# Performance work log

Hardware: AMD Instinct MI355X
Metric: run time of the kernel (lower is better)

## Reference

```python
import jax, jax.numpy as jnp
from jax import lax
import numpy as np
import math

N, T, H, PD = 1024, 32, 256, 256
E, DT, SD = 2 * H, H // 16, 16  # mamba expand, dt_rank, state_dim
TAU = 1.0

def _xavier(k, shape):
    s = math.sqrt(6.0 / (shape[0] + shape[1]))
    return jax.random.uniform(k, shape, minval=-s, maxval=s, dtype=jnp.float32)

def setup_inputs() -> dict:
    key = jax.random.key(0)
    ks = jax.random.split(key, 40)
    adj = (jax.random.uniform(ks[0], (T, N, N)) < 0.02).astype(jnp.float32)
    p = {
        'adj': adj,
        # input SpatialLayer (pos_dim -> H)
        'msg1_w': _xavier(ks[1], (PD, H)), 'msg1_b': jnp.zeros(H),
        'upd1_w': _xavier(ks[2], (PD + H, H)), 'upd1_b': jnp.zeros(H),
        'ln1_g': jnp.ones(H), 'ln1_b': jnp.zeros(H),
        # second SpatialLayer (H -> H)
        'msg2_w': _xavier(ks[3], (H, H)), 'msg2_b': jnp.zeros(H),
        'upd2_w': _xavier(ks[4], (2 * H, H)), 'upd2_b': jnp.zeros(H),
        'ln2_g': jnp.ones(H), 'ln2_b': jnp.zeros(H),
        # MambaBlock
        'mb_ln_g': jnp.ones(H), 'mb_ln_b': jnp.zeros(H),
        'in_w': _xavier(ks[5], (H, 2 * E)), 'in_b': jnp.zeros(2 * E),
        'delta_w': _xavier(ks[6], (E, DT)), 'delta_b': jnp.zeros(DT),
        'dt_w': _xavier(ks[7], (DT, E)), 'dt_b': jnp.zeros(E),
        'Bp_w': _xavier(ks[8], (E, SD)), 'Bp_b': jnp.zeros(SD),
        'Cp_w': _xavier(ks[9], (E, SD)), 'Cp_b': jnp.zeros(SD),
        'A_log': -jnp.exp(0.1 * jax.random.normal(ks[10], (E, SD))),
        'D_vec': jnp.zeros(E),
        'out_w': _xavier(ks[11], (E, H)), 'out_b': jnp.zeros(H),
        # LateEdgeGateHead
        'q_w': _xavier(ks[12], (H, H)), 'k_w': _xavier(ks[13], (H, H)),
        'gate_bias': jnp.float32(-1.0),
    }
    return p

def _layernorm(x, g, b, eps=1e-5):
    mu = jnp.mean(x, -1, keepdims=True)
    var = jnp.mean(jnp.square(x - mu), -1, keepdims=True)
    return (x - mu) / jnp.sqrt(var + eps) * g + b

def _sincos_pe(n, d):
    pos = jnp.arange(n, dtype=jnp.float32)[:, None]
    div = jnp.exp(jnp.arange(0, d, 2, dtype=jnp.float32) * (-math.log(10000.0) / d))
    ang = pos * div  # [n, d/2]
    return jnp.stack([jnp.sin(ang), jnp.cos(ang)], axis=-1).reshape(n, d)

def reference(adj, msg1_w, msg1_b, upd1_w, upd1_b, ln1_g, ln1_b,
              msg2_w, msg2_b, upd2_w, upd2_b, ln2_g, ln2_b,
              mb_ln_g, mb_ln_b, in_w, in_b, delta_w, delta_b, dt_w, dt_b,
              Bp_w, Bp_b, Cp_w, Cp_b, A_log, D_vec, out_w, out_b,
              q_w, k_w, gate_bias):
    pe = _sincos_pe(N, PD)  # [N, PD]
    # --- spatial layer 1 (shared pe across time) ---
    m1 = pe @ msg1_w + msg1_b                                   # [N, H]
    agg1 = jnp.einsum('tij,jh->tih', adj, m1)                   # [T, N, H]
    x = jnp.concatenate([jnp.broadcast_to(pe, (T, N, PD)), agg1], -1)
    x = _layernorm(jax.nn.relu(x @ upd1_w + upd1_b), ln1_g, ln1_b)
    # --- spatial layer 2 ---
    m2 = x @ msg2_w + msg2_b
    agg2 = jnp.einsum('tij,tjh->tih', adj, m2)
    x = jnp.concatenate([x, agg2], -1)
    x = _layernorm(jax.nn.relu(x @ upd2_w + upd2_b), ln2_g, ln2_b)  # [T, N, H]
    # --- Mamba over time, batch = nodes ---
    seq = jnp.transpose(x, (1, 0, 2))                           # [N, T, H]
    res = seq
    xn = _layernorm(seq, mb_ln_g, mb_ln_b)
    xp = xn @ in_w + in_b
    x1, gate = jnp.split(xp, 2, axis=-1)                        # [N, T, E] each
    x1 = jax.nn.silu(x1)
    delta = jax.nn.softplus((x1 @ delta_w + delta_b) @ dt_w + dt_b)  # [N, T, E]
    Bm = x1 @ Bp_w + Bp_b                                       # [N, T, SD]
    Cm = x1 @ Cp_w + Cp_b
    A = -jnp.exp(A_log)                                         # [E, SD]
    def step(h, inp):
        xt, dt_, bt, ct = inp                                   # [N,E],[N,E],[N,SD],[N,SD]
        A_disc = jnp.exp(dt_[:, :, None] * A)                   # [N, E, SD]
        h = A_disc * h + dt_[:, :, None] * bt[:, None, :] * xt[:, :, None]
        yt = jnp.sum(ct[:, None, :] * h, -1)                    # [N, E]
        return h, yt
    h0 = jnp.zeros((N, E, SD), dtype=seq.dtype)
    xs = (jnp.swapaxes(x1, 0, 1), jnp.swapaxes(delta, 0, 1),
          jnp.swapaxes(Bm, 0, 1), jnp.swapaxes(Cm, 0, 1))
    _, ys = lax.scan(step, h0, xs)                              # [T, N, E]
    y = jnp.swapaxes(ys, 0, 1) + x1 * D_vec
    y = y * jax.nn.silu(gate)
    mb_out = y @ out_w + out_b + res                            # [N, T, H]
    outs = jnp.transpose(mb_out, (1, 0, 2))                     # [T, N, H]
    # --- late gate head per timestep ---
    q = outs @ q_w
    k = outs @ k_w
    scores = jnp.einsum('tnh,tmh->tnm', q, k) / (math.sqrt(H) * max(TAU, 1e-6))
    logits = scores + gate_bias
    probs = jax.nn.sigmoid(logits)
    return outs, probs, logits
```

## Files before the change

### kernel.cpp

```cpp
#include <hip/hip_runtime.h>
#include <hip/hip_bf16.h>

typedef __hip_bfloat16 bf16;
typedef short s16x8 __attribute__((ext_vector_type(8)));
typedef float f32x4 __attribute__((ext_vector_type(4)));

#define T_  32
#define N_  1024
#define H_  256
#define E_  512
#define SD_ 16

static const long MBYTE = 1024L * 1024L;

__device__ __forceinline__ float b2f(bf16 v){ return __bfloat162float(v); }
__device__ __forceinline__ bf16  f2b(float v){ return __float2bfloat16(v); }
__device__ __forceinline__ void  stf(bf16* p, float v){ *p = f2b(v); }
__device__ __forceinline__ void  stf(float* p, float v){ *p = v; }

#define G2L16(gp, lp) __builtin_amdgcn_global_load_lds( \
    (const __attribute__((address_space(1))) void*)(const void*)(gp), \
    (__attribute__((address_space(3))) void*)(void*)(lp), 16, 0, 0)

struct TDesc { const float* src; int K; int N; bf16* dst; int ldT; };
struct PrepArgs {
    TDesc t[13];
    bf16* pe;
    const float* pa; const float* pb; const float* pc; float* po;
};

__global__ __launch_bounds__(256) void prep_kernel(PrepArgs P){
    int z = blockIdx.z;
    int tid = threadIdx.x;
    if (z < 13) {
        const TDesc d = P.t[z];
        int k0 = blockIdx.x * 32, n0 = blockIdx.y * 32;
        if (k0 >= d.K || n0 >= d.N) return;
        __shared__ float S[32][33];
        int r = tid >> 3, c4 = (tid & 7) * 4;
        #pragma unroll
        for (int u = 0; u < 4; ++u) {
            int k = k0 + r, n = n0 + c4 + u;
            S[r][c4 + u] = (k < d.K && n < d.N) ? d.src[(long)k * d.N + n] : 0.0f;
        }
        __syncthreads();
        int n = n0 + (tid >> 3);
        #pragma unroll
        for (int u = 0; u < 4; ++u) {
            int k = k0 + (tid & 7) * 4 + u;
            if (n < d.N && k < d.K) d.dst[(long)n * d.ldT + k] = f2b(S[(tid & 7) * 4 + u][tid >> 3]);
        }
    } else if (z == 13) {
        int n = blockIdx.y * 32 + blockIdx.x;
        int dd = tid;
        int i2 = (dd >> 1) * 2;
        float div = __expf((float)i2 * (-9.210340371976184f / 256.0f));
        float ang = (float)n * div;
        P.pe[n * 256 + dd] = f2b((dd & 1) ? __cosf(ang) : __sinf(ang));
    } else {
        if (blockIdx.x || blockIdx.y) return;
        if (tid < 16) P.po[tid] = P.pa[tid];
        else if (tid < 32) P.po[tid] = P.pb[tid - 16];
        else if (tid < 48) P.po[tid] = P.pc[tid - 32];
    }
}

template<int OP>
__global__ __launch_bounds__(256) void mfma_gemm128(
    const bf16* __restrict__ A, int lda,
    const bf16* BT0, const bf16* BT1, int ldbt0, int ldbt1,
    float* Cf0, float* Cf1, bf16* Cb0, bf16* Cb1, int ldc,
    int K, const float* bias0, const float* bias1, const float* res)
{
    int z = blockIdx.z;
    const bf16* BT = z ? BT1 : BT0;
    int ldbt = z ? ldbt1 : ldbt0;
    float* Cf = z ? Cf1 : Cf0;
    bf16*  Cb = z ? Cb1 : Cb0;
    const float* bias = z ? bias1 : bias0;

    __shared__ short As[4096];
    __shared__ short Bs[4096];
    int tid = threadIdx.x;
    int w = tid >> 6, l = tid & 63;
    int wr = w >> 1, wc = w & 1;
    long row0 = (long)blockIdx.y * 128, col0 = (long)blockIdx.x * 128;
    const short* Ag = (const short*)A + row0 * lda;
    const short* Bg = (const short*)BT + col0 * ldbt;
    int sr = w * 16 + (l >> 2);
    int sc = (l & 3) * 8;
    short* lA = As + w * 512 + l * 8;
    short* lB = Bs + w * 512 + l * 8;
    f32x4 acc[4][4] = {};
    for (int k0 = 0; k0 < K; k0 += 32) {
        G2L16(Ag + (long)sr * lda + k0 + sc, lA);
        G2L16(Ag + (long)(sr + 64) * lda + k0 + sc, lA + 2048);
        G2L16(Bg + (long)sr * ldbt + k0 + sc, lB);
        G2L16(Bg + (long)(sr + 64) * ldbt + k0 + sc, lB + 2048);
        __syncthreads();
        s16x8 af[4], bf[4];
        #pragma unroll
        for (int f = 0; f < 4; ++f) {
            af[f] = *(const s16x8*)&As[(wr * 64 + f * 16 + (l & 15)) * 32 + (l >> 4) * 8];
            bf[f] = *(const s16x8*)&Bs[(wc * 64 + f * 16 + (l & 15)) * 32 + (l >> 4) * 8];
        }
        #pragma unroll
        for (int fm = 0; fm < 4; ++fm)
            #pragma unroll
            for (int fn = 0; fn < 4; ++fn)
                acc[fm][fn] = __builtin_amdgcn_mfma_f32_16x16x32_bf16(af[fm], bf[fn], acc[fm][fn], 0, 0, 0);
        __syncthreads();
    }
    #pragma unroll
    for (int fm = 0; fm < 4; ++fm) {
        int er = (int)row0 + wr * 64 + fm * 16 + (l >> 4) * 4;
        #pragma unroll
        for (int fn = 0; fn < 4; ++fn) {
            int ec = (int)col0 + wc * 64 + fn * 16 + (l & 15);
            float bb = bias ? bias[ec] : 0.0f;
            #pragma unroll
            for (int rg = 0; rg < 4; ++rg) {
                long idx = (long)(er + rg) * ldc + ec;
                float v = acc[fm][fn][rg] + bb;
                if (res) v += res[idx];
                if (OP == 1) v = v / (1.0f + __expf(-v));
                if (Cf) Cf[idx] = v;
                if (Cb) Cb[idx] = f2b(v);
            }
        }
    }
}

__global__ __launch_bounds__(256) void score_mfma128(
    const bf16* __restrict__ Q, const bf16* __restrict__ Km,
    float* __restrict__ probs, float* __restrict__ logits,
    const float* __restrict__ gbp)
{
    int t = blockIdx.z;
    const short* Ag = (const short*)(Q  + (long)t * N_ * 256) + (long)blockIdx.y * 128 * 256;
    const short* Bg = (const short*)(Km + (long)t * N_ * 256) + (long)blockIdx.x * 128 * 256;
    __shared__ short As[4096];
    __shared__ short Bs[4096];
    int tid = threadIdx.x;
    int w = tid >> 6, l = tid & 63;
    int wr = w >> 1, wc = w & 1;
    int sr = w * 16 + (l >> 2);
    int sc = (l & 3) * 8;
    short* lA = As + w * 512 + l * 8;
    short* lB = Bs + w * 512 + l * 8;
    f32x4 acc[4][4] = {};
    for (int k0 = 0; k0 < 256; k0 += 32) {
        G2L16(Ag + (long)sr * 256 + k0 + sc, lA);
        G2L16(Ag + (long)(sr + 64) * 256 + k0 + sc, lA + 2048);
        G2L16(Bg + (long)sr * 256 + k0 + sc, lB);
        G2L16(Bg + (long)(sr + 64) * 256 + k0 + sc, lB + 2048);
        __syncthreads();
        s16x8 af[4], bf[4];
        #pragma unroll
        for (int f = 0; f < 4; ++f) {
            af[f] = *(const s16x8*)&As[(wr * 64 + f * 16 + (l & 15)) * 32 + (l >> 4) * 8];
            bf[f] = *(const s16x8*)&Bs[(wc * 64 + f * 16 + (l & 15)) * 32 + (l >> 4) * 8];
        }
        #pragma unroll
        for (int fm = 0; fm < 4; ++fm)
            #pragma unroll
            for (int fn = 0; fn < 4; ++fn)
                acc[fm][fn] = __builtin_amdgcn_mfma_f32_16x16x32_bf16(af[fm], bf[fn], acc[fm][fn], 0, 0, 0);
        __syncthreads();
    }
    float gb = gbp[0];
    long tbase = (long)t * N_ * N_;
    int row0 = blockIdx.y * 128, col0 = blockIdx.x * 128;
    #pragma unroll
    for (int fm = 0; fm < 4; ++fm) {
        int er = row0 + wr * 64 + fm * 16 + (l >> 4) * 4;
        #pragma unroll
        for (int fn = 0; fn < 4; ++fn) {
            int ec = col0 + wc * 64 + fn * 16 + (l & 15);
            #pragma unroll
            for (int rg = 0; rg < 4; ++rg) {
                float zz = acc[fm][fn][rg] * 0.0625f + gb;
                long idx = tbase + (long)(er + rg) * N_ + ec;
                logits[idx] = zz;
                probs[idx]  = 1.0f / (1.0f + __expf(-zz));
            }
        }
    }
}

__global__ __launch_bounds__(256) void mfma_gemm64(
    const bf16* __restrict__ A, int lda,
    const bf16* __restrict__ BT, int ldbt,
    float* __restrict__ Cf, int ldc,
    int M, int N, int K, const float* __restrict__ bias)
{
    __shared__ short As[64][40];
    __shared__ short Bs[64][40];
    int tid = threadIdx.x;
    int w = tid >> 6, l = tid & 63;
    int row0 = blockIdx.y * 64, col0 = blockIdx.x * 64;
    int sr = tid >> 2, sk = (tid & 3) * 8;
    const short* Ag = (const short*)A;
    const short* Bg = (const short*)BT;
    f32x4 acc[4] = {};
    for (int k0 = 0; k0 < K; k0 += 32) {
        *(s16x8*)&As[sr][sk] = *(const s16x8*)(Ag + (long)(row0 + sr) * lda + k0 + sk);
        int bn = col0 + sr;
        s16x8 bv = {};
        if (bn < N) bv = *(const s16x8*)(Bg + (long)bn * ldbt + k0 + sk);
        *(s16x8*)&Bs[sr][sk] = bv;
        __syncthreads();
        s16x8 a = *(const s16x8*)&As[w * 16 + (l & 15)][(l >> 4) * 8];
        #pragma unroll
        for (int ct = 0; ct < 4; ++ct) {
            s16x8 b = *(const s16x8*)&Bs[ct * 16 + (l & 15)][(l >> 4) * 8];
            acc[ct] = __builtin_amdgcn_mfma_f32_16x16x32_bf16(a, b, acc[ct], 0, 0, 0);
        }
        __syncthreads();
    }
    int er = row0 + w * 16 + (l >> 4) * 4;
    int ec = l & 15;
    #pragma unroll
    for (int ct = 0; ct < 4; ++ct) {
        int gc = col0 + ct * 16 + ec;
        if (gc >= N) continue;
        float bb = bias ? bias[gc] : 0.0f;
        #pragma unroll
        for (int rg = 0; rg < 4; ++rg)
            Cf[(long)(er + rg) * ldc + gc] = acc[ct][rg] + bb;
    }
}

__global__ __launch_bounds__(256) void idx_build(
    const float* __restrict__ adj, unsigned short* __restrict__ IDX, int* __restrict__ CNT)
{
    int r = blockIdx.x;
    const float* arow = adj + ((long)r << 10);
    __shared__ int wcnt[4];
    int tid = threadIdx.x, wv = tid >> 6, lane = tid & 63;
    int total = 0;
    unsigned short* out = IDX + (long)r * 128;
    #pragma unroll
    for (int u = 0; u < 4; ++u) {
        float av = arow[u * 256 + tid];
        unsigned long long mask = __ballot(av != 0.0f);
        if (lane == 0) wcnt[wv] = __popcll(mask);
        __syncthreads();
        int base = total;
        for (int w2 = 0; w2 < wv; ++w2) base += wcnt[w2];
        if (av != 0.0f) {
            int pos = base + __popcll(mask & ((1ull << lane) - 1ull));
            if (pos < 128) out[pos] = (unsigned short)(u * 256 + tid);
        }
        total += wcnt[0] + wcnt[1] + wcnt[2] + wcnt[3];
        __syncthreads();
    }
    if (tid == 0) CNT[r] = total < 128 ? total : 128;
}

__global__ __launch_bounds__(256) void agg_gather(
    const unsigned short* __restrict__ IDX, const int* __restrict__ CNT,
    const bf16* __restrict__ Bm, long tstride,
    bf16* __restrict__ out, int old, int ooff)
{
    int r = blockIdx.x;
    int t = r >> 10;
    const bf16* B = Bm + (long)t * tstride;
    __shared__ unsigned short sidx[128];
    int tid = threadIdx.x;
    int cnt = CNT[r];
    if (tid < 128) sidx[tid] = IDX[(long)r * 128 + tid];
    __syncthreads();
    float acc = 0.0f;
    for (int k = 0; k < cnt; ++k)
        acc += b2f(B[(long)sidx[k] * 256 + tid]);
    out[(long)r * old + ooff + tid] = f2b(acc);
}

__global__ __launch_bounds__(256) void row_ln1(
    const float* __restrict__ in, const float* __restrict__ addf,
    const float* __restrict__ g, const float* __restrict__ b,
    bf16* __restrict__ out, int rows)
{
    int wv = threadIdx.x >> 6, lane = threadIdx.x & 63;
    int row = blockIdx.x * 4 + wv;
    if (row >= rows) return;
    const float* p = in + (long)row * 256 + lane * 4;
    const float* q = addf + (long)(row & 1023) * 256 + lane * 4;
    float v[4];
    #pragma unroll
    for (int u = 0; u < 4; ++u) v[u] = fmaxf(p[u] + q[u], 0.0f);
    float s = v[0] + v[1] + v[2] + v[3];
    #pragma unroll
    for (int o = 32; o >= 1; o >>= 1) s += __shfl_xor(s, o, 64);
    float mu = s * (1.0f / 256.0f);
    float d0 = v[0]-mu, d1 = v[1]-mu, d2 = v[2]-mu, d3 = v[3]-mu;
    float sq = d0*d0 + d1*d1 + d2*d2 + d3*d3;
    #pragma unroll
    for (int o = 32; o >= 1; o >>= 1) sq += __shfl_xor(sq, o, 64);
    float rs = rsqrtf(sq * (1.0f / 256.0f) + 1e-5f);
    bf16* o = out + (long)row * 512 + lane * 4;
    #pragma unroll
    for (int u = 0; u < 4; ++u)
        o[u] = f2b((v[u] - mu) * rs * g[lane * 4 + u] + b[lane * 4 + u]);
}

__global__ __launch_bounds__(256) void dbl_ln(
    const float* __restrict__ in,
    const float* __restrict__ g2, const float* __restrict__ b2,
    const float* __restrict__ gm, const float* __restrict__ bm,
    float* __restrict__ X2f, bf16* __restrict__ XNb, int rows)
{
    int wv = threadIdx.x >> 6, lane = threadIdx.x & 63;
    int row = blockIdx.x * 4 + wv;
    if (row >= rows) return;
    const float* p = in + (long)row * 256 + lane * 4;
    float v[4];
    #pragma unroll
    for (int u = 0; u < 4; ++u) v[u] = fmaxf(p[u], 0.0f);
    float s = v[0] + v[1] + v[2] + v[3];
    #pragma unroll
    for (int o = 32; o >= 1; o >>= 1) s += __shfl_xor(s, o, 64);
    float mu = s * (1.0f / 256.0f);
    float sq = 0.0f;
    #pragma unroll
    for (int u = 0; u < 4; ++u) { float d = v[u] - mu; sq += d * d; }
    #pragma unroll
    for (int o = 32; o >= 1; o >>= 1) sq += __shfl_xor(sq, o, 64);
    float rs = rsqrtf(sq * (1.0f / 256.0f) + 1e-5f);
    float o1[4];
    float* qx = X2f + (long)row * 256 + lane * 4;
    #pragma unroll
    for (int u = 0; u < 4; ++u) {
        o1[u] = (v[u] - mu) * rs * g2[lane * 4 + u] + b2[lane * 4 + u];
        qx[u] = o1[u];
    }
    float s2 = o1[0] + o1[1] + o1[2] + o1[3];
    #pragma unroll
    for (int o = 32; o >= 1; o >>= 1) s2 += __shfl_xor(s2, o, 64);
    float mu2 = s2 * (1.0f / 256.0f);
    float sq2 = 0.0f;
    #pragma unroll
    for (int u = 0; u < 4; ++u) { float d = o1[u] - mu2; sq2 += d * d; }
    #pragma unroll
    for (int o = 32; o >= 1; o >>= 1) sq2 += __shfl_xor(sq2, o, 64);
    float rs2 = rsqrtf(sq2 * (1.0f / 256.0f) + 1e-5f);
    bf16* qn = XNb + (long)row * 256 + lane * 4;
    #pragma unroll
    for (int u = 0; u < 4; ++u)
        qn[u] = f2b((o1[u] - mu2) * rs2 * gm[lane * 4 + u] + bm[lane * 4 + u]);
}

__global__ __launch_bounds__(512) void scan2(
    const bf16* __restrict__ X1,
    bf16* __restrict__ G,
    const float* __restrict__ DBC,
    const bf16* __restrict__ DTwT,
    const float* __restrict__ DTb,
    const float* __restrict__ A_log,
    const float* __restrict__ D_vec)
{
    int n = blockIdx.x;
    int e = threadIdx.x;
    float A[SD_], wdt[SD_];
    #pragma unroll
    for (int s = 0; s < SD_; ++s) A[s] = -__expf(A_log[e * SD_ + s]);
    #pragma unroll
    for (int s = 0; s < SD_; ++s) wdt[s] = b2f(DTwT[e * SD_ + s]);
    float dtb = DTb[e];
    float Dv = D_vec[e];
    float h[SD_];
    #pragma unroll
    for (int s = 0; s < SD_; ++s) h[s] = 0.0f;
    for (int t = 0; t < T_; ++t) {
        long row = (long)t * N_ + n;
        const float* dbc = DBC + row * 48;
        float z = dtb;
        #pragma unroll
        for (int k = 0; k < SD_; ++k) z += dbc[k] * wdt[k];
        float dt = (z > 15.0f) ? z : __logf(1.0f + __expf(z));
        float x1 = b2f(X1[row * (long)E_ + e]);
        float gv = b2f(G[row * (long)E_ + e]);
        float dx = dt * x1;
        float yv = 0.0f;
        #pragma unroll
        for (int s = 0; s < SD_; ++s) {
            h[s] = __expf(dt * A[s]) * h[s] + dx * dbc[16 + s];
            yv += dbc[32 + s] * h[s];
        }
        G[row * (long)E_ + e] = f2b((yv + x1 * Dv) * gv);
    }
}

extern "C" void kernel_launch(void* const* d_in, const int* in_sizes, int n_in,
                              void* d_out, int out_size, void* d_ws, size_t ws_size,
                              hipStream_t stream)
{
    if (ws_size < (size_t)(212 * MBYTE)) return;
    if (n_in != 32 || in_sizes[0] != T_ * N_ * N_ || in_sizes[15] != 256 * 1024) return;

    const float* adj = (const float*)d_in[0];
    const float* P1w = (const float*)d_in[1];
    const float* P1b = (const float*)d_in[2];
    const float* U1w = (const float*)d_in[3];
    const float* U1b = (const float*)d_in[4];
    const float* L1g = (const float*)d_in[5];
    const float* L1b = (const float*)d_in[6];
    const float* P2w = (const float*)d_in[7];
    const float* P2b = (const float*)d_in[8];
    const float* U2w = (const float*)d_in[9];
    const float* U2b = (const float*)d_in[10];
    const float* L2g = (const float*)d_in[11];
    const float* L2b = (const float*)d_in[12];
    const float* MBg = (const float*)d_in[13];
    const float* MBb = (const float*)d_in[14];
    const float* INw = (const float*)d_in[15];
    const float* INb = (const float*)d_in[16];
    const float* DLw = (const float*)d_in[17];
    const float* DLb = (const float*)d_in[18];
    const float* DTw = (const float*)d_in[19];
    const float* DTb = (const float*)d_in[20];
    const float* BPw = (const float*)d_in[21];
    const float* BPb = (const float*)d_in[22];
    const float* CPw = (const float*)d_in[23];
    const float* CPb = (const float*)d_in[24];
    const float* ALg = (const float*)d_in[25];
    const float* DV  = (const float*)d_in[26];
    const float* OWw = (const float*)d_in[27];
    const float* OWb = (const float*)d_in[28];
    const float* QWw = (const float*)d_in[29];
    const float* KWw = (const float*)d_in[30];
    const float* GB  = (const float*)d_in[31];

    char* w = (char*)d_ws;
    float* R0    = (float*)(w + 0);
    bf16*  XCATb = (bf16*)(w + 32 * MBYTE);
    bf16*  AGG1b = (bf16*)(w + 64 * MBYTE);
    bf16*  M2b   = (bf16*)(w + 64 * MBYTE);
    bf16*  OUTb  = (bf16*)(w + 64 * MBYTE);
    bf16*  X1b   = (bf16*)(w + 80 * MBYTE);
    bf16*  Gb    = (bf16*)(w + 112 * MBYTE);
    float* X2f   = (float*)(w + 144 * MBYTE);
    bf16*  Qb    = (bf16*)(w + 144 * MBYTE);
    bf16*  Kb    = (bf16*)(w + 160 * MBYTE);
    bf16*  XNb   = (bf16*)(w + 176 * MBYTE);
    float* DBC   = (float*)(w + 192 * MBYTE);
    unsigned short* IDX = (unsigned short*)(w + 198 * MBYTE);
    int*   CNT   = (int*)(w + 206 * MBYTE);
    float* BASE1 = (float*)(w + 207 * MBYTE);
    bf16*  PEb   = (bf16*)(w + 208 * MBYTE);
    bf16*  M1b   = (bf16*)(w + 208 * MBYTE + 524288);
    bf16*  WT    = (bf16*)(w + 209 * MBYTE);
    float* B48   = (float*)(w + 211 * MBYTE);

    bf16* P1wT  = WT + 0;
    bf16* U1wT  = WT + 65536;
    bf16* P2wT  = WT + 196608;
    bf16* U2wT  = WT + 262144;
    bf16* INwT  = WT + 393216;
    bf16* DTwT  = WT + 655360;
    bf16* OWwT  = WT + 663552;
    bf16* QWwT  = WT + 794624;
    bf16* KWwT  = WT + 860160;
    bf16* DBCwT = WT + 925696;

    float* out0       = (float*)d_out;
    float* out_probs  = out0 + (long)T_ * N_ * H_;
    float* out_logits = out_probs + (long)T_ * N_ * N_;

    const int RN = T_ * N_;
    dim3 blk(256);
    const float* fnull = nullptr;
    float* f32null = nullptr;
    bf16*  b16null = nullptr;

    PrepArgs P;
    P.t[0]  = {P1w, 256, 256,  P1wT, 256};
    P.t[1]  = {U1w, 512, 256,  U1wT, 512};
    P.t[2]  = {P2w, 256, 256,  P2wT, 256};
    P.t[3]  = {U2w, 512, 256,  U2wT, 512};
    P.t[4]  = {INw, 256, 1024, INwT, 256};
    P.t[5]  = {DTw, 16,  512,  DTwT, 16};
    P.t[6]  = {OWw, 512, 256,  OWwT, 512};
    P.t[7]  = {QWw, 256, 256,  QWwT, 256};
    P.t[8]  = {KWw, 256, 256,  KWwT, 256};
    P.t[9]  = {DLw, 512, 16,   DBCwT, 512};
    P.t[10] = {BPw, 512, 16,   DBCwT + 16 * 512, 512};
    P.t[11] = {CPw, 512, 16,   DBCwT + 32 * 512, 512};
    P.t[12] = {DLw, 1,   1,    DBCwT, 512};
    P.pe = PEb; P.pa = DLb; P.pb = BPb; P.pc = CPb; P.po = B48;
    hipLaunchKernelGGL(prep_kernel, dim3(32, 32, 15), blk, 0, stream, P);
    hipLaunchKernelGGL(idx_build, dim3(RN), blk, 0, stream, adj, IDX, CNT);

    hipLaunchKernelGGL((mfma_gemm128<0>), dim3(2, 8, 2), blk, 0, stream,
                       PEb, 256, P1wT, U1wT, 256, 512,
                       f32null, BASE1, M1b, b16null, 256, 256, P1b, U1b, fnull);

    hipLaunchKernelGGL(agg_gather, dim3(RN), blk, 0, stream, IDX, CNT, M1b, 0L, AGG1b, 256, 0);

    hipLaunchKernelGGL((mfma_gemm128<0>), dim3(2, 256, 1), blk, 0, stream,
                       AGG1b, 256, U1wT + 256, U1wT + 256, 512, 512,
                       R0, f32null, b16null, b16null, 256, 256, fnull, fnull, fnull);
    hipLaunchKernelGGL(row_ln1, dim3(RN / 4), blk, 0, stream, R0, BASE1, L1g, L1b, XCATb, RN);

    hipLaunchKernelGGL((mfma_gemm128<0>), dim3(2, 256, 1), blk, 0, stream,
                       XCATb, 512, P2wT, P2wT, 256, 256,
                       f32null, f32null, M2b, b16null, 256, 256, P2b, fnull, fnull);

    hipLaunchKernelGGL(agg_gather, dim3(RN), blk, 0, stream, IDX, CNT, M2b,
                       (long)N_ * 256, XCATb, 512, 256);

    hipLaunchKernelGGL((mfma_gemm128<0>), dim3(2, 256, 1), blk, 0, stream,
                       XCATb, 512, U2wT, U2wT, 512, 512,
                       R0, f32null, b16null, b16null, 256, 512, U2b, fnull, fnull);
    hipLaunchKernelGGL(dbl_ln, dim3(RN / 4), blk, 0, stream,
                       R0, L2g, L2b, MBg, MBb, X2f, XNb, RN);

    hipLaunchKernelGGL((mfma_gemm128<1>), dim3(4, 256, 2), blk, 0, stream,
                       XNb, 256, INwT, INwT + 512 * 256, 256, 256,
                       f32null, f32null, X1b, Gb, 512, 256, INb, INb + 512, fnull);

    hipLaunchKernelGGL(mfma_gemm64, dim3(1, 512), blk, 0, stream,
                       X1b, 512, DBCwT, 512, DBC, 48, RN, 48, 512, B48);

    hipLaunchKernelGGL(scan2, dim3(N_), dim3(512), 0, stream,
                       X1b, Gb, DBC, DTwT, DTb, ALg, DV);

    hipLaunchKernelGGL((mfma_gemm128<0>), dim3(2, 256, 1), blk, 0, stream,
                       Gb, 512, OWwT, OWwT, 512, 512,
                       out0, f32null, OUTb, b16null, 256, 512, OWb, fnull, X2f);

    hipLaunchKernelGGL((mfma_gemm128<0>), dim3(2, 256, 2), blk, 0, stream,
                       OUTb, 256, QWwT, KWwT, 256, 256,
                       f32null, f32null, Qb, Kb, 256, 256, fnull, fnull, fnull);

    hipLaunchKernelGGL(score_mfma128, dim3(8, 8, T_), blk, 0, stream,
                       Qb, Kb, out_probs, out_logits, GB);
}
```

Before: 582.3 us.

## Merge index build into prep kernel, unroll gather, use nontemporal logit stores

```diff
diff --git a/kernel.cpp b/kernel.cpp
--- a/kernel.cpp
+++ b/kernel.cpp
@@ -15,8 +15,6 @@
 
 __device__ __forceinline__ float b2f(bf16 v){ return __bfloat162float(v); }
 __device__ __forceinline__ bf16  f2b(float v){ return __float2bfloat16(v); }
-__device__ __forceinline__ void  stf(bf16* p, float v){ *p = f2b(v); }
-__device__ __forceinline__ void  stf(float* p, float v){ *p = v; }
 
 #define G2L16(gp, lp) __builtin_amdgcn_global_load_lds( \
     (const __attribute__((address_space(1))) void*)(const void*)(gp), \
@@ -27,6 +25,7 @@
     TDesc t[13];
     bf16* pe;
     const float* pa; const float* pb; const float* pc; float* po;
+    const float* adj; unsigned short* IDX; int* CNT;
 };
 
 __global__ __launch_bounds__(256) void prep_kernel(PrepArgs P){
@@ -57,11 +56,34 @@
         float div = __expf((float)i2 * (-9.210340371976184f / 256.0f));
         float ang = (float)n * div;
         P.pe[n * 256 + dd] = f2b((dd & 1) ? __cosf(ang) : __sinf(ang));
-    } else {
+    } else if (z == 14) {
         if (blockIdx.x || blockIdx.y) return;
         if (tid < 16) P.po[tid] = P.pa[tid];
         else if (tid < 32) P.po[tid] = P.pb[tid - 16];
         else if (tid < 48) P.po[tid] = P.pc[tid - 32];
+    } else {
+        int r = (z - 15) * 1024 + blockIdx.y * 32 + blockIdx.x;
+        const float* arow = P.adj + ((long)r << 10);
+        __shared__ int wcnt[4];
+        int wv = tid >> 6, lane = tid & 63;
+        int total = 0;
+        unsigned short* out = P.IDX + (long)r * 128;
+        #pragma unroll
+        for (int u = 0; u < 4; ++u) {
+            float av = arow[u * 256 + tid];
+            unsigned long long mask = __ballot(av != 0.0f);
+            if (lane == 0) wcnt[wv] = __popcll(mask);
+            __syncthreads();
+            int base = total;
+            for (int w2 = 0; w2 < wv; ++w2) base += wcnt[w2];
+            if (av != 0.0f) {
+                int pos = base + __popcll(mask & ((1ull << lane) - 1ull));
+                if (pos < 128) out[pos] = (unsigned short)(u * 256 + tid);
+            }
+            total += wcnt[0] + wcnt[1] + wcnt[2] + wcnt[3];
+            __syncthreads();
+        }
+        if (tid == 0) P.CNT[r] = total < 128 ? total : 128;
     }
 }
 
@@ -181,8 +203,8 @@
             for (int rg = 0; rg < 4; ++rg) {
                 float zz = acc[fm][fn][rg] * 0.0625f + gb;
                 long idx = tbase + (long)(er + rg) * N_ + ec;
-                logits[idx] = zz;
-                probs[idx]  = 1.0f / (1.0f + __expf(-zz));
+                __builtin_nontemporal_store(zz, &logits[idx]);
+                __builtin_nontemporal_store(1.0f / (1.0f + __expf(-zz)), &probs[idx]);
             }
         }
     }
@@ -231,33 +253,6 @@
     }
 }
 
-__global__ __launch_bounds__(256) void idx_build(
-    const float* __restrict__ adj, unsigned short* __restrict__ IDX, int* __restrict__ CNT)
-{
-    int r = blockIdx.x;
-    const float* arow = adj + ((long)r << 10);
-    __shared__ int wcnt[4];
-    int tid = threadIdx.x, wv = tid >> 6, lane = tid & 63;
-    int total = 0;
-    unsigned short* out = IDX + (long)r * 128;
-    #pragma unroll
-    for (int u = 0; u < 4; ++u) {
-        float av = arow[u * 256 + tid];
-        unsigned long long mask = __ballot(av != 0.0f);
-        if (lane == 0) wcnt[wv] = __popcll(mask);
-        __syncthreads();
-        int base = total;
-        for (int w2 = 0; w2 < wv; ++w2) base += wcnt[w2];
-        if (av != 0.0f) {
-            int pos = base + __popcll(mask & ((1ull << lane) - 1ull));
-            if (pos < 128) out[pos] = (unsigned short)(u * 256 + tid);
-        }
-        total += wcnt[0] + wcnt[1] + wcnt[2] + wcnt[3];
-        __syncthreads();
-    }
-    if (tid == 0) CNT[r] = total < 128 ? total : 128;
-}
-
 __global__ __launch_bounds__(256) void agg_gather(
     const unsigned short* __restrict__ IDX, const int* __restrict__ CNT,
     const bf16* __restrict__ Bm, long tstride,
@@ -271,10 +266,17 @@
     int cnt = CNT[r];
     if (tid < 128) sidx[tid] = IDX[(long)r * 128 + tid];
     __syncthreads();
-    float acc = 0.0f;
-    for (int k = 0; k < cnt; ++k)
-        acc += b2f(B[(long)sidx[k] * 256 + tid]);
-    out[(long)r * old + ooff + tid] = f2b(acc);
+    float a0 = 0.0f, a1 = 0.0f, a2 = 0.0f, a3 = 0.0f;
+    int k = 0;
+    for (; k + 4 <= cnt; k += 4) {
+        float v0 = b2f(B[(long)sidx[k]     * 256 + tid]);
+        float v1 = b2f(B[(long)sidx[k + 1] * 256 + tid]);
+        float v2 = b2f(B[(long)sidx[k + 2] * 256 + tid]);
+        float v3 = b2f(B[(long)sidx[k + 3] * 256 + tid]);
+        a0 += v0; a1 += v1; a2 += v2; a3 += v3;
+    }
+    for (; k < cnt; ++k) a0 += b2f(B[(long)sidx[k] * 256 + tid]);
+    out[(long)r * old + ooff + tid] = f2b((a0 + a1) + (a2 + a3));
 }
 
 __global__ __launch_bounds__(256) void row_ln1(
@@ -489,8 +491,8 @@
     P.t[11] = {CPw, 512, 16,   DBCwT + 32 * 512, 512};
     P.t[12] = {DLw, 1,   1,    DBCwT, 512};
     P.pe = PEb; P.pa = DLb; P.pb = BPb; P.pc = CPb; P.po = B48;
-    hipLaunchKernelGGL(prep_kernel, dim3(32, 32, 15), blk, 0, stream, P);
-    hipLaunchKernelGGL(idx_build, dim3(RN), blk, 0, stream, adj, IDX, CNT);
+    P.adj = adj; P.IDX = IDX; P.CNT = CNT;
+    hipLaunchKernelGGL(prep_kernel, dim3(32, 32, 47), blk, 0, stream, P);
 
     hipLaunchKernelGGL((mfma_gemm128<0>), dim3(2, 8, 2), blk, 0, stream,
                        PEb, 256, P1wT, U1wT, 256, 512,
```

After: 565.2 us. -2.9%, faster.
